# Kernel optimization log

Hardware: AMD Instinct MI355X
Metric: run time of the kernel (lower is better)

Reference implementation:

```python
import jax, jax.numpy as jnp
import numpy as np

N_NODES = 100000
N_EDGES = 600000
IN_DIM = 128
HID = 128
OUT_DIM = 64
N_LAYERS = 3


def setup_inputs() -> dict:
    key = jax.random.key(0)
    ks = jax.random.split(key, 8)
    x = jax.random.normal(ks[0], (N_NODES, IN_DIM), dtype=jnp.float32)
    edge_index = jax.random.randint(ks[1], (2, N_EDGES), 0, N_NODES, dtype=jnp.int64)
    s = 1.0 / np.sqrt(HID)
    W_in = jax.random.normal(ks[2], (HID, IN_DIM), dtype=jnp.float32) * s
    b_in = jax.random.normal(ks[3], (HID,), dtype=jnp.float32) * s
    W_convs = jax.random.normal(ks[4], (N_LAYERS, HID, HID), dtype=jnp.float32) * s
    b_convs = jax.random.normal(ks[5], (N_LAYERS, HID), dtype=jnp.float32) * s
    W_out = jax.random.normal(ks[6], (OUT_DIM, (N_LAYERS + 1) * HID), dtype=jnp.float32) * s
    b_out = jax.random.normal(ks[7], (OUT_DIM,), dtype=jnp.float32) * s
    return {"x": x, "edge_index": edge_index, "W_in": W_in, "b_in": b_in,
            "W_convs": W_convs, "b_convs": b_convs, "W_out": W_out, "b_out": b_out}


def reference(x, edge_index, W_in, b_in, W_convs, b_convs, W_out, b_out):
    src, dst = edge_index[0], edge_index[1]
    n = x.shape[0]
    # input projection: [N, in] -> [N, H]
    h = x @ W_in.T + b_in
    hidden_states = [h]
    for i in range(W_convs.shape[0]):
        # GINConv (eps=0): nn(x + sum of neighbor messages), messages src->dst
        agg = jax.ops.segment_sum(h[src], dst, num_segments=n)
        h = (h + agg) @ W_convs[i].T + b_convs[i]
        hidden_states.append(h)
    cat = jnp.concatenate(hidden_states, axis=1)  # [N, (L+1)*H]
    out = cat @ W_out.T + b_out  # [N, OUT]
    return jax.nn.softmax(out, axis=-1)
```

## Files before the change

### kernel.cpp

```cpp
#include <hip/hip_runtime.h>
#include <hip/hip_bf16.h>
#include <hip/hip_fp16.h>

#define GN 100000
#define GE 600000
#define SCAN_NBLK 98
#define ALD 132

typedef __bf16    bf16x8 __attribute__((ext_vector_type(8)));
typedef __bf16    bf16x4 __attribute__((ext_vector_type(4)));
typedef _Float16  f16x8  __attribute__((ext_vector_type(8)));
typedef float     f32x4  __attribute__((ext_vector_type(4)));

__global__ __launch_bounds__(256) void convert_w(
    const float* __restrict__ Win, const float* __restrict__ Wc,
    const float* __restrict__ Wout,
    __bf16* __restrict__ hi, __bf16* __restrict__ lo)
{
    const int i = blockIdx.x * 256 + threadIdx.x;
    if (i >= 98304) return;
    float v;
    if (i < 16384)      v = Win[i];
    else if (i < 65536) v = Wc[i - 16384];
    else                v = Wout[i - 65536];
    const __bf16 h = (__bf16)v;
    hi[i] = h;
    lo[i] = (__bf16)(v - (float)h);
}

__global__ __launch_bounds__(256, 8) void gather_rows(
    const uint* __restrict__ Hw,
    const int* __restrict__ row_start,
    const int* __restrict__ deg,
    const int* __restrict__ csr,
    float* __restrict__ Agg)
{
    const int wave = threadIdx.x >> 6;
    const int lane = threadIdx.x & 63;
    const int row  = blockIdx.x * 4 + wave;
    if (row >= GN) return;

    const int start = row_start[row];
    const int dg    = deg[row];
    float2 acc = make_float2(0.f, 0.f);

    for (int b = 0; b < dg; b += 64) {
        const int n = min(dg - b, 64);
        const int idx = csr[start + min(b + lane, dg - 1)];
        for (int k = 0; k < n; k += 8) {
            uint t[8];
#pragma unroll
            for (int u = 0; u < 8; ++u) {
                const int s = __shfl(idx, min(k + u, n - 1));
                t[u] = Hw[(size_t)s * 64 + lane];
            }
            const int m = min(n - k, 8);
#pragma unroll
            for (int u = 0; u < 8; ++u) {
                if (u < m) {
                    union { uint uu; _Float16 h[2]; } cv;
                    cv.uu = t[u];
                    acc.x += (float)cv.h[0];
                    acc.y += (float)cv.h[1];
                }
            }
        }
    }
    *(float2*)&Agg[(size_t)row * 128 + lane * 2] = acc;
}

template<bool HASAGG>
__global__ __launch_bounds__(256, 3) void gin_layer(
    const float* __restrict__ H, int ldH,
    const float* __restrict__ Agg,
    const __bf16* __restrict__ Whi,
    const __bf16* __restrict__ Wlo,
    const float* __restrict__ bias,
    float* __restrict__ C, int ldC,
    _Float16* __restrict__ HfOut)
{
    __shared__ float Acc[32 * ALD];

    const int tid  = threadIdx.x;
    const int wave = tid >> 6;
    const int lane = tid & 63;
    const int row0 = blockIdx.x * 32;
    const int wn   = wave * 32;
    const int quad = lane >> 4;
    const int l15  = lane & 15;

    {
        const int c = (lane & 31) * 4;
        f32x4 sv[4];
#pragma unroll
        for (int p = 0; p < 4; ++p) {
            const int r = wave * 8 + p * 2 + (lane >> 5);
            sv[p] = *(const f32x4*)(H + (size_t)(row0 + r) * ldH + c);
            if (HASAGG)
                sv[p] += *(const f32x4*)(Agg + (size_t)(row0 + r) * 128 + c);
        }
#pragma unroll
        for (int p = 0; p < 4; ++p) {
            const int r = wave * 8 + p * 2 + (lane >> 5);
            *(f32x4*)&Acc[r * ALD + c] = sv[p];
        }
    }
    __syncthreads();

    f32x4 acc[2][2];
#pragma unroll
    for (int i = 0; i < 2; ++i)
#pragma unroll
        for (int j = 0; j < 2; ++j) acc[i][j] = (f32x4)(0.0f);

    bf16x8 whA[2], wlA[2], whB[2], wlB[2];
#pragma unroll
    for (int nt = 0; nt < 2; ++nt) {
        const int n = wn + nt * 16 + l15;
        whA[nt] = *(const bf16x8*)(Whi + (size_t)n * 128 + quad * 8);
        wlA[nt] = *(const bf16x8*)(Wlo + (size_t)n * 128 + quad * 8);
    }

#pragma unroll
    for (int ks = 0; ks < 4; ++ks) {
        const int kt = ks * 32 + quad * 8;
        if (ks < 3) {
            const int kn = kt + 32;
#pragma unroll
            for (int nt = 0; nt < 2; ++nt) {
                const int n = wn + nt * 16 + l15;
                whB[nt] = *(const bf16x8*)(Whi + (size_t)n * 128 + kn);
                wlB[nt] = *(const bf16x8*)(Wlo + (size_t)n * 128 + kn);
            }
        }
        bf16x8 ahi[2], alo[2];
#pragma unroll
        for (int mt = 0; mt < 2; ++mt) {
            const float* ap = &Acc[(mt * 16 + l15) * ALD + kt];
            const f32x4 p = *(const f32x4*)ap;
            const f32x4 q = *(const f32x4*)(ap + 4);
#pragma unroll
            for (int e = 0; e < 4; ++e) {
                const __bf16 hp = (__bf16)p[e];
                const __bf16 hq = (__bf16)q[e];
                ahi[mt][e]     = hp;
                ahi[mt][e + 4] = hq;
                alo[mt][e]     = (__bf16)(p[e] - (float)hp);
                alo[mt][e + 4] = (__bf16)(q[e] - (float)hq);
            }
        }
#pragma unroll
        for (int mt = 0; mt < 2; ++mt)
#pragma unroll
            for (int nt = 0; nt < 2; ++nt) {
                acc[mt][nt] = __builtin_amdgcn_mfma_f32_16x16x32_bf16(
                    ahi[mt], whA[nt], acc[mt][nt], 0, 0, 0);
                acc[mt][nt] = __builtin_amdgcn_mfma_f32_16x16x32_bf16(
                    ahi[mt], wlA[nt], acc[mt][nt], 0, 0, 0);
                acc[mt][nt] = __builtin_amdgcn_mfma_f32_16x16x32_bf16(
                    alo[mt], whA[nt], acc[mt][nt], 0, 0, 0);
            }
        if (ks < 3) {
#pragma unroll
            for (int nt = 0; nt < 2; ++nt) {
                whA[nt] = whB[nt];
                wlA[nt] = wlB[nt];
            }
        }
    }
    __syncthreads();

#pragma unroll
    for (int nt = 0; nt < 2; ++nt) {
        const int col = wn + nt * 16 + l15;
        const float b = bias[col];
#pragma unroll
        for (int mt = 0; mt < 2; ++mt)
#pragma unroll
            for (int r4 = 0; r4 < 4; ++r4)
                Acc[(mt * 16 + quad * 4 + r4) * ALD + col] = acc[mt][nt][r4] + b;
    }
    __syncthreads();
#pragma unroll
    for (int p = 0; p < 4; ++p) {
        const int q  = tid + p * 256;
        const int r  = q >> 5;
        const int c4 = (q & 31) * 4;
        *(float4*)(C + (size_t)(row0 + r) * ldC + c4) = *(const float4*)&Acc[r * ALD + c4];
    }
#pragma unroll
    for (int p = 0; p < 2; ++p) {
        const int q = tid + p * 256;
        const int r = q >> 4;
        const int g = (q & 15) * 8;
        const float4 a = *(const float4*)&Acc[r * ALD + g];
        const float4 b = *(const float4*)&Acc[r * ALD + g + 4];
        f16x8 o = {(_Float16)a.x, (_Float16)a.y, (_Float16)a.z, (_Float16)a.w,
                   (_Float16)b.x, (_Float16)b.y, (_Float16)b.z, (_Float16)b.w};
        *(f16x8*)&HfOut[(size_t)(row0 + r) * 128 + g] = o;
    }
}

__global__ __launch_bounds__(256, 3) void gin_final(
    const float* __restrict__ cat3,
    const float* __restrict__ Agg,
    const __bf16* __restrict__ Whi3,
    const __bf16* __restrict__ Wlo3,
    const float* __restrict__ b3,
    const __bf16* __restrict__ WhiO,
    const __bf16* __restrict__ WloO,
    const float* __restrict__ bO,
    float* __restrict__ out)
{
    constexpr int CLD = 68;

    __shared__ float Smem[32 * ALD];
    float* const Acc = Smem;
    float* const Cst = Smem;

    const int tid  = threadIdx.x;
    const int wave = tid >> 6;
    const int lane = tid & 63;
    const int row0 = blockIdx.x * 32;
    const int quad = lane >> 4;
    const int l15  = lane & 15;

    {
        const int c = (lane & 31) * 4;
        f32x4 sv[4];
#pragma unroll
        for (int p = 0; p < 4; ++p) {
            const int r = wave * 8 + p * 2 + (lane >> 5);
            sv[p] = *(const f32x4*)(cat3 + (size_t)(row0 + r) * 384 + 256 + c);
            sv[p] += *(const f32x4*)(Agg + (size_t)(row0 + r) * 128 + c);
        }
#pragma unroll
        for (int p = 0; p < 4; ++p) {
            const int r = wave * 8 + p * 2 + (lane >> 5);
            *(f32x4*)&Acc[r * ALD + c] = sv[p];
        }
    }
    __syncthreads();

    const int wn = wave * 32;
    f32x4 acc1[2][2];
#pragma unroll
    for (int i = 0; i < 2; ++i)
#pragma unroll
        for (int j = 0; j < 2; ++j) acc1[i][j] = (f32x4)(0.0f);

    {
        bf16x8 whA[2], wlA[2], whB[2], wlB[2];
#pragma unroll
        for (int nt = 0; nt < 2; ++nt) {
            const int n = wn + nt * 16 + l15;
            whA[nt] = *(const bf16x8*)(Whi3 + (size_t)n * 128 + quad * 8);
            wlA[nt] = *(const bf16x8*)(Wlo3 + (size_t)n * 128 + quad * 8);
        }
#pragma unroll
        for (int ks = 0; ks < 4; ++ks) {
            const int kt = ks * 32 + quad * 8;
            if (ks < 3) {
                const int kn = kt + 32;
#pragma unroll
                for (int nt = 0; nt < 2; ++nt) {
                    const int n = wn + nt * 16 + l15;
                    whB[nt] = *(const bf16x8*)(Whi3 + (size_t)n * 128 + kn);
                    wlB[nt] = *(const bf16x8*)(Wlo3 + (size_t)n * 128 + kn);
                }
            }
            bf16x8 ahi[2], alo[2];
#pragma unroll
            for (int mt = 0; mt < 2; ++mt) {
                const float* ap = &Acc[(mt * 16 + l15) * ALD + kt];
                const f32x4 p = *(const f32x4*)ap;
                const f32x4 q = *(const f32x4*)(ap + 4);
#pragma unroll
                for (int e = 0; e < 4; ++e) {
                    const __bf16 hp = (__bf16)p[e];
                    const __bf16 hq = (__bf16)q[e];
                    ahi[mt][e]     = hp;
                    ahi[mt][e + 4] = hq;
                    alo[mt][e]     = (__bf16)(p[e] - (float)hp);
                    alo[mt][e + 4] = (__bf16)(q[e] - (float)hq);
                }
            }
#pragma unroll
            for (int mt = 0; mt < 2; ++mt)
#pragma unroll
                for (int nt = 0; nt < 2; ++nt) {
                    acc1[mt][nt] = __builtin_amdgcn_mfma_f32_16x16x32_bf16(
                        ahi[mt], whA[nt], acc1[mt][nt], 0, 0, 0);
                    acc1[mt][nt] = __builtin_amdgcn_mfma_f32_16x16x32_bf16(
                        ahi[mt], wlA[nt], acc1[mt][nt], 0, 0, 0);
                    acc1[mt][nt] = __builtin_amdgcn_mfma_f32_16x16x32_bf16(
                        alo[mt], whA[nt], acc1[mt][nt], 0, 0, 0);
                }
            if (ks < 3) {
#pragma unroll
                for (int nt = 0; nt < 2; ++nt) {
                    whA[nt] = whB[nt];
                    wlA[nt] = wlB[nt];
                }
            }
        }
    }
    __syncthreads();

#pragma unroll
    for (int nt = 0; nt < 2; ++nt) {
        const int col = wn + nt * 16 + l15;
        const float b = b3[col];
#pragma unroll
        for (int mt = 0; mt < 2; ++mt)
#pragma unroll
            for (int r4 = 0; r4 < 4; ++r4)
                Acc[(mt * 16 + quad * 4 + r4) * ALD + col] = acc1[mt][nt][r4] + b;
    }
    __syncthreads();

    const int wk  = wave & 1;
    const int wn2 = (wave >> 1) * 32;
    f32x4 acc2[2][2];
#pragma unroll
    for (int i = 0; i < 2; ++i)
#pragma unroll
        for (int j = 0; j < 2; ++j) acc2[i][j] = (f32x4)(0.0f);

    f32x4 pA[2], qA[2], pB[2], qB[2];
    bf16x8 whA[2], wlA[2], whB[2], wlB[2];

    {
        const int kg = wk * 256 + quad * 8;
#pragma unroll
        for (int mt = 0; mt < 2; ++mt) {
            const int row = mt * 16 + l15;
            const float* ap = cat3 + (size_t)(row0 + row) * 384 + kg;
            pA[mt] = *(const f32x4*)ap;
            qA[mt] = *(const f32x4*)(ap + 4);
        }
#pragma unroll
        for (int nt = 0; nt < 2; ++nt) {
            const int n = wn2 + nt * 16 + l15;
            whA[nt] = *(const bf16x8*)(WhiO + (size_t)n * 512 + kg);
            wlA[nt] = *(const bf16x8*)(WloO + (size_t)n * 512 + kg);
        }
    }

#pragma unroll
    for (int ks = 0; ks < 8; ++ks) {
        if (ks < 7) {
            const int kg = wk * 256 + (ks + 1) * 32 + quad * 8;
#pragma unroll
            for (int mt = 0; mt < 2; ++mt) {
                const int row = mt * 16 + l15;
                if (kg < 384) {
                    const float* ap = cat3 + (size_t)(row0 + row) * 384 + kg;
                    pB[mt] = *(const f32x4*)ap;
                    qB[mt] = *(const f32x4*)(ap + 4);
                } else {
                    const float* ap = &Acc[row * ALD + (kg - 384)];
                    pB[mt] = *(const f32x4*)ap;
                    qB[mt] = *(const f32x4*)(ap + 4);
                }
            }
#pragma unroll
            for (int nt = 0; nt < 2; ++nt) {
                const int n = wn2 + nt * 16 + l15;
                whB[nt] = *(const bf16x8*)(WhiO + (size_t)n * 512 + kg);
                wlB[nt] = *(const bf16x8*)(WloO + (size_t)n * 512 + kg);
            }
        }
        bf16x8 ahi[2], alo[2];
#pragma unroll
        for (int mt = 0; mt < 2; ++mt) {
#pragma unroll
            for (int e = 0; e < 4; ++e) {
                const __bf16 hp = (__bf16)pA[mt][e];
                const __bf16 hq = (__bf16)qA[mt][e];
                ahi[mt][e]     = hp;
                ahi[mt][e + 4] = hq;
                alo[mt][e]     = (__bf16)(pA[mt][e] - (float)hp);
                alo[mt][e + 4] = (__bf16)(qA[mt][e] - (float)hq);
            }
        }
#pragma unroll
        for (int mt = 0; mt < 2; ++mt)
#pragma unroll
            for (int nt = 0; nt < 2; ++nt) {
                acc2[mt][nt] = __builtin_amdgcn_mfma_f32_16x16x32_bf16(
                    ahi[mt], whA[nt], acc2[mt][nt], 0, 0, 0);
                acc2[mt][nt] = __builtin_amdgcn_mfma_f32_16x16x32_bf16(
                    ahi[mt], wlA[nt], acc2[mt][nt], 0, 0, 0);
                acc2[mt][nt] = __builtin_amdgcn_mfma_f32_16x16x32_bf16(
                    alo[mt], whA[nt], acc2[mt][nt], 0, 0, 0);
            }
        if (ks < 7) {
#pragma unroll
            for (int mt = 0; mt < 2; ++mt) { pA[mt] = pB[mt]; qA[mt] = qB[mt]; }
#pragma unroll
            for (int nt = 0; nt < 2; ++nt) { whA[nt] = whB[nt]; wlA[nt] = wlB[nt]; }
        }
    }

    __syncthreads();

    if (wk == 1) {
#pragma unroll
        for (int nt = 0; nt < 2; ++nt)
#pragma unroll
            for (int mt = 0; mt < 2; ++mt)
#pragma unroll
                for (int r4 = 0; r4 < 4; ++r4)
                    Cst[(mt * 16 + quad * 4 + r4) * CLD + wn2 + nt * 16 + l15]
                        = acc2[mt][nt][r4];
    }
    __syncthreads();
    if (wk == 0) {
#pragma unroll
        for (int nt = 0; nt < 2; ++nt) {
            const int col = wn2 + nt * 16 + l15;
            const float b = bO[col];
#pragma unroll
            for (int mt = 0; mt < 2; ++mt)
#pragma unroll
                for (int r4 = 0; r4 < 4; ++r4) {
                    const int idx = (mt * 16 + quad * 4 + r4) * CLD + col;
                    Cst[idx] = Cst[idx] + acc2[mt][nt][r4] + b;
                }
        }
    }
    __syncthreads();

    for (int i = 0; i < 8; ++i) {
        const int r = wave * 8 + i;
        const float v = Cst[r * CLD + lane];
        float m = v;
#pragma unroll
        for (int off = 32; off > 0; off >>= 1) m = fmaxf(m, __shfl_xor(m, off));
        const float e = __expf(v - m);
        float s = e;
#pragma unroll
        for (int off = 32; off > 0; off >>= 1) s += __shfl_xor(s, off);
        out[(size_t)(row0 + r) * 64 + lane] = e / s;
    }
}

__global__ __launch_bounds__(256) void count_deg(const int* __restrict__ dst,
                                                 int* __restrict__ deg)
{
    const int e = blockIdx.x * 256 + threadIdx.x;
    if (e < GE) atomicAdd(&deg[dst[e]], 1);
}

__global__ __launch_bounds__(256) void scan_pass1(const int* __restrict__ deg,
                                                  int* __restrict__ excl,
                                                  int* __restrict__ blockSums)
{
    __shared__ int s[256];
    const int t = threadIdx.x;
    const int base = blockIdx.x * 1024 + t * 4;

    int4 v = make_int4(0, 0, 0, 0);
    if (base + 3 < GN) {
        v = *(const int4*)(deg + base);
    } else {
        if (base + 0 < GN) v.x = deg[base + 0];
        if (base + 1 < GN) v.y = deg[base + 1];
        if (base + 2 < GN) v.z = deg[base + 2];
        if (base + 3 < GN) v.w = deg[base + 3];
    }
    const int mysum = v.x + v.y + v.z + v.w;
    s[t] = mysum;
    __syncthreads();
    for (int off = 1; off < 256; off <<= 1) {
        const int val = (t >= off) ? s[t - off] : 0;
        __syncthreads();
        s[t] += val;
        __syncthreads();
    }
    int4 o;
    o.x = s[t] - mysum;
    o.y = o.x + v.x;
    o.z = o.y + v.y;
    o.w = o.z + v.z;
    if (base + 3 < GN) {
        *(int4*)(excl + base) = o;
    } else {
        if (base + 0 < GN) excl[base + 0] = o.x;
        if (base + 1 < GN) excl[base + 1] = o.y;
        if (base + 2 < GN) excl[base + 2] = o.z;
        if (base + 3 < GN) excl[base + 3] = o.w;
    }
    if (t == 255) blockSums[blockIdx.x] = s[255];
}

__global__ __launch_bounds__(128) void scan_pass2(const int* __restrict__ blockSums,
                                                  int* __restrict__ blockOffs, int n)
{
    __shared__ int s[128];
    const int t = threadIdx.x;
    const int v = (t < n) ? blockSums[t] : 0;
    s[t] = v;
    __syncthreads();
    for (int off = 1; off < 128; off <<= 1) {
        const int val = (t >= off) ? s[t - off] : 0;
        __syncthreads();
        s[t] += val;
        __syncthreads();
    }
    if (t < n) blockOffs[t] = s[t] - v;
}

__global__ __launch_bounds__(256) void scan_pass3(int* __restrict__ excl,
                                                  const int* __restrict__ blockOffs,
                                                  int* __restrict__ cursor)
{
    const int i = blockIdx.x * 256 + threadIdx.x;
    if (i >= GN) return;
    const int v = excl[i] + blockOffs[i >> 10];
    excl[i]   = v;
    cursor[i] = v;
}

__global__ __launch_bounds__(256) void fill_csr(const int* __restrict__ src,
                                                const int* __restrict__ dst,
                                                int* __restrict__ cursor,
                                                int* __restrict__ csr)
{
    const int e = blockIdx.x * 256 + threadIdx.x;
    if (e >= GE) return;
    const int pos = atomicAdd(&cursor[dst[e]], 1);
    csr[pos] = src[e];
}

extern "C" void kernel_launch(void* const* d_in, const int* in_sizes, int n_in,
                              void* d_out, int out_size, void* d_ws, size_t ws_size,
                              hipStream_t stream)
{
    const float* x       = (const float*)d_in[0];
    const int*   src     = (const int*)d_in[1];
    const int*   dst     = ((const int*)d_in[1]) + GE;
    const float* W_in    = (const float*)d_in[2];
    const float* b_in    = (const float*)d_in[3];
    const float* W_convs = (const float*)d_in[4];
    const float* b_convs = (const float*)d_in[5];
    const float* W_out   = (const float*)d_in[6];
    const float* b_out   = (const float*)d_in[7];
    float*       out     = (float*)d_out;

    float*    cat3 = (float*)d_ws;
    _Float16* Hf   = (_Float16*)(cat3 + (size_t)GN * 384);
    float*    Agg  = (float*)(Hf + (size_t)GN * 128);
    int*      deg       = (int*)(Agg + (size_t)GN * 128);
    int*      row_start = deg + GN;
    int*      cursor    = row_start + GN;
    int*      blockSums = cursor + GN;
    int*      blockOffs = blockSums + 128;
    int*      csr       = blockOffs + 128;
    __bf16*   Whi       = (__bf16*)(csr + GE);
    __bf16*   Wlo       = Whi + 98304;

    const dim3 blk(256);
    const dim3 gblk(256);
    const int edge_blocks   = (GE + 255) / 256;
    const int node_blocks   = (GN + 255) / 256;
    const int layer_blocks  = GN / 32;
    const int gather_blocks = (GN + 3) / 4;

    hipMemsetAsync(deg, 0, GN * sizeof(int), stream);
    count_deg<<<edge_blocks, blk, 0, stream>>>(dst, deg);
    scan_pass1<<<SCAN_NBLK, blk, 0, stream>>>(deg, row_start, blockSums);
    scan_pass2<<<1, 128, 0, stream>>>(blockSums, blockOffs, SCAN_NBLK);
    scan_pass3<<<node_blocks, blk, 0, stream>>>(row_start, blockOffs, cursor);
    fill_csr<<<edge_blocks, blk, 0, stream>>>(src, dst, cursor, csr);

    convert_w<<<(98304 + 255) / 256, blk, 0, stream>>>(W_in, W_convs, W_out, Whi, Wlo);

    gin_layer<false><<<layer_blocks, gblk, 0, stream>>>(
        x, 128, nullptr, Whi, Wlo, b_in, cat3, 384, Hf);

    gather_rows<<<gather_blocks, gblk, 0, stream>>>(
        (const uint*)Hf, row_start, deg, csr, Agg);
    gin_layer<true><<<layer_blocks, gblk, 0, stream>>>(
        cat3, 384, Agg, Whi + 16384, Wlo + 16384, b_convs, cat3 + 128, 384, Hf);

    gather_rows<<<gather_blocks, gblk, 0, stream>>>(
        (const uint*)Hf, row_start, deg, csr, Agg);
    gin_layer<true><<<layer_blocks, gblk, 0, stream>>>(
        cat3 + 128, 384, Agg, Whi + 32768, Wlo + 32768, b_convs + 128,
        cat3 + 256, 384, Hf);

    gather_rows<<<gather_blocks, gblk, 0, stream>>>(
        (const uint*)Hf, row_start, deg, csr, Agg);
    gin_final<<<layer_blocks, gblk, 0, stream>>>(
        cat3, Agg, Whi + 49152, Wlo + 49152, b_convs + 256,
        Whi + 65536, Wlo + 65536, b_out, out);
}
```

Baseline: 499.3 us.

## Process two 32-row tiles per block in gin_layer with prefetched second tile

Each gin_layer block now handles 64 rows as two 32-row tiles with double-buffered shared memory. Global loads for the second tile are issued up front so they overlap with the first tile's MFMA work, and the first tile's epilogue is interleaved with the second GEMM. The GEMM body moves into a shared inline helper that gin_final also calls. In exchange, shared memory and register use per block roughly double, which may reduce occupancy, and the grid becomes half as many blocks with a bounds guard for the tail.

Result: slower. 513.5 us (+2.8%).

```diff
diff --git a/kernel.cpp b/kernel.cpp
--- a/kernel.cpp
+++ b/kernel.cpp
@@ -69,6 +69,73 @@
     *(float2*)&Agg[(size_t)row * 128 + lane * 2] = acc;
 }
 
+__device__ __forceinline__ void gemm_tile(
+    const float* __restrict__ AccBuf,
+    const __bf16* __restrict__ Whi, const __bf16* __restrict__ Wlo,
+    const int wn, const int quad, const int l15,
+    f32x4 acc[2][2])
+{
+#pragma unroll
+    for (int i = 0; i < 2; ++i)
+#pragma unroll
+        for (int j = 0; j < 2; ++j) acc[i][j] = (f32x4)(0.0f);
+
+    bf16x8 whA[2], wlA[2], whB[2], wlB[2];
+#pragma unroll
+    for (int nt = 0; nt < 2; ++nt) {
+        const int n = wn + nt * 16 + l15;
+        whA[nt] = *(const bf16x8*)(Whi + (size_t)n * 128 + quad * 8);
+        wlA[nt] = *(const bf16x8*)(Wlo + (size_t)n * 128 + quad * 8);
+    }
+#pragma unroll
+    for (int ks = 0; ks < 4; ++ks) {
+        const int kt = ks * 32 + quad * 8;
+        if (ks < 3) {
+            const int kn = kt + 32;
+#pragma unroll
+            for (int nt = 0; nt < 2; ++nt) {
+                const int n = wn + nt * 16 + l15;
+                whB[nt] = *(const bf16x8*)(Whi + (size_t)n * 128 + kn);
+                wlB[nt] = *(const bf16x8*)(Wlo + (size_t)n * 128 + kn);
+            }
+        }
+        bf16x8 ahi[2], alo[2];
+#pragma unroll
+        for (int mt = 0; mt < 2; ++mt) {
+            const float* ap = &AccBuf[(mt * 16 + l15) * ALD + kt];
+            const f32x4 p = *(const f32x4*)ap;
+            const f32x4 q = *(const f32x4*)(ap + 4);
+#pragma unroll
+            for (int e = 0; e < 4; ++e) {
+                const __bf16 hp = (__bf16)p[e];
+                const __bf16 hq = (__bf16)q[e];
+                ahi[mt][e]     = hp;
+                ahi[mt][e + 4] = hq;
+                alo[mt][e]     = (__bf16)(p[e] - (float)hp);
+                alo[mt][e + 4] = (__bf16)(q[e] - (float)hq);
+            }
+        }
+#pragma unroll
+        for (int mt = 0; mt < 2; ++mt)
+#pragma unroll
+            for (int nt = 0; nt < 2; ++nt) {
+                acc[mt][nt] = __builtin_amdgcn_mfma_f32_16x16x32_bf16(
+                    ahi[mt], whA[nt], acc[mt][nt], 0, 0, 0);
+                acc[mt][nt] = __builtin_amdgcn_mfma_f32_16x16x32_bf16(
+                    ahi[mt], wlA[nt], acc[mt][nt], 0, 0, 0);
+                acc[mt][nt] = __builtin_amdgcn_mfma_f32_16x16x32_bf16(
+                    alo[mt], whA[nt], acc[mt][nt], 0, 0, 0);
+            }
+        if (ks < 3) {
+#pragma unroll
+            for (int nt = 0; nt < 2; ++nt) {
+                whA[nt] = whB[nt];
+                wlA[nt] = wlB[nt];
+            }
+        }
+    }
+}
+
 template<bool HASAGG>
 __global__ __launch_bounds__(256, 3) void gin_layer(
     const float* __restrict__ H, int ldH,
@@ -79,94 +146,50 @@
     float* __restrict__ C, int ldC,
     _Float16* __restrict__ HfOut)
 {
-    __shared__ float Acc[32 * ALD];
+    __shared__ float Acc[2][32 * ALD];
 
     const int tid  = threadIdx.x;
     const int wave = tid >> 6;
     const int lane = tid & 63;
-    const int row0 = blockIdx.x * 32;
+    const int row0 = blockIdx.x * 64;
     const int wn   = wave * 32;
     const int quad = lane >> 4;
     const int l15  = lane & 15;
-
-    {
-        const int c = (lane & 31) * 4;
-        f32x4 sv[4];
-#pragma unroll
-        for (int p = 0; p < 4; ++p) {
-            const int r = wave * 8 + p * 2 + (lane >> 5);
-            sv[p] = *(const f32x4*)(H + (size_t)(row0 + r) * ldH + c);
-            if (HASAGG)
-                sv[p] += *(const f32x4*)(Agg + (size_t)(row0 + r) * 128 + c);
-        }
-#pragma unroll
-        for (int p = 0; p < 4; ++p) {
-            const int r = wave * 8 + p * 2 + (lane >> 5);
-            *(f32x4*)&Acc[r * ALD + c] = sv[p];
-        }
-    }
-    __syncthreads();
-
-    f32x4 acc[2][2];
-#pragma unroll
-    for (int i = 0; i < 2; ++i)
-#pragma unroll
-        for (int j = 0; j < 2; ++j) acc[i][j] = (f32x4)(0.0f);
-
-    bf16x8 whA[2], wlA[2], whB[2], wlB[2];
-#pragma unroll
-    for (int nt = 0; nt < 2; ++nt) {
-        const int n = wn + nt * 16 + l15;
-        whA[nt] = *(const bf16x8*)(Whi + (size_t)n * 128 + quad * 8);
-        wlA[nt] = *(const bf16x8*)(Wlo + (size_t)n * 128 + quad * 8);
-    }
-
-#pragma unroll
-    for (int ks = 0; ks < 4; ++ks) {
-        const int kt = ks * 32 + quad * 8;
-        if (ks < 3) {
-            const int kn = kt + 32;
-#pragma unroll
-            for (int nt = 0; nt < 2; ++nt) {
-                const int n = wn + nt * 16 + l15;
-                whB[nt] = *(const bf16x8*)(Whi + (size_t)n * 128 + kn);
-                wlB[nt] = *(const bf16x8*)(Wlo + (size_t)n * 128 + kn);
-            }
-        }
-        bf16x8 ahi[2], alo[2];
-#pragma unroll
-        for (int mt = 0; mt < 2; ++mt) {
-            const float* ap = &Acc[(mt * 16 + l15) * ALD + kt];
-            const f32x4 p = *(const f32x4*)ap;
-            const f32x4 q = *(const f32x4*)(ap + 4);
-#pragma unroll
-            for (int e = 0; e < 4; ++e) {
-                const __bf16 hp = (__bf16)p[e];
-                const __bf16 hq = (__bf16)q[e];
-                ahi[mt][e]     = hp;
-                ahi[mt][e + 4] = hq;
-                alo[mt][e]     = (__bf16)(p[e] - (float)hp);
-                alo[mt][e + 4] = (__bf16)(q[e] - (float)hq);
-            }
-        }
-#pragma unroll
-        for (int mt = 0; mt < 2; ++mt)
-#pragma unroll
-            for (int nt = 0; nt < 2; ++nt) {
-                acc[mt][nt] = __builtin_amdgcn_mfma_f32_16x16x32_bf16(
-                    ahi[mt], whA[nt], acc[mt][nt], 0, 0, 0);
-                acc[mt][nt] = __builtin_amdgcn_mfma_f32_16x16x32_bf16(
-                    ahi[mt], wlA[nt], acc[mt][nt], 0, 0, 0);
-                acc[mt][nt] = __builtin_amdgcn_mfma_f32_16x16x32_bf16(
-                    alo[mt], whA[nt], acc[mt][nt], 0, 0, 0);
-            }
-        if (ks < 3) {
-#pragma unroll
-            for (int nt = 0; nt < 2; ++nt) {
-                whA[nt] = whB[nt];
-                wlA[nt] = wlB[nt];
-            }
-        }
+    const int c    = (lane & 31) * 4;
+    const int hp2  = lane >> 5;
+
+    f32x4 s0[4], a0[4], s1[4], a1[4];
+#pragma unroll
+    for (int p = 0; p < 4; ++p) {
+        const int r0 = min(row0 + wave * 8 + p * 2 + hp2, GN - 1);
+        s0[p] = *(const f32x4*)(H + (size_t)r0 * ldH + c);
+        if (HASAGG) a0[p] = *(const f32x4*)(Agg + (size_t)r0 * 128 + c);
+    }
+#pragma unroll
+    for (int p = 0; p < 4; ++p) {
+        const int r1 = min(row0 + 32 + wave * 8 + p * 2 + hp2, GN - 1);
+        s1[p] = *(const f32x4*)(H + (size_t)r1 * ldH + c);
+        if (HASAGG) a1[p] = *(const f32x4*)(Agg + (size_t)r1 * 128 + c);
+    }
+
+#pragma unroll
+    for (int p = 0; p < 4; ++p) {
+        const int r = wave * 8 + p * 2 + hp2;
+        f32x4 v = s0[p];
+        if (HASAGG) v += a0[p];
+        *(f32x4*)&Acc[0][r * ALD + c] = v;
+    }
+    __syncthreads();
+
+    f32x4 acc0[2][2];
+    gemm_tile(Acc[0], Whi, Wlo, wn, quad, l15, acc0);
+
+#pragma unroll
+    for (int p = 0; p < 4; ++p) {
+        const int r = wave * 8 + p * 2 + hp2;
+        f32x4 v = s1[p];
+        if (HASAGG) v += a1[p];
+        *(f32x4*)&Acc[1][r * ALD + c] = v;
     }
     __syncthreads();
 
@@ -178,26 +201,71 @@
         for (int mt = 0; mt < 2; ++mt)
 #pragma unroll
             for (int r4 = 0; r4 < 4; ++r4)
-                Acc[(mt * 16 + quad * 4 + r4) * ALD + col] = acc[mt][nt][r4] + b;
-    }
-    __syncthreads();
+                Acc[0][(mt * 16 + quad * 4 + r4) * ALD + col] = acc0[mt][nt][r4] + b;
+    }
+
+    f32x4 acc1[2][2];
+    gemm_tile(Acc[1], Whi, Wlo, wn, quad, l15, acc1);
+    __syncthreads();
+
 #pragma unroll
     for (int p = 0; p < 4; ++p) {
         const int q  = tid + p * 256;
         const int r  = q >> 5;
         const int c4 = (q & 31) * 4;
-        *(float4*)(C + (size_t)(row0 + r) * ldC + c4) = *(const float4*)&Acc[r * ALD + c4];
+        const int gr = row0 + r;
+        if (gr < GN)
+            *(float4*)(C + (size_t)gr * ldC + c4) = *(const float4*)&Acc[0][r * ALD + c4];
     }
 #pragma unroll
     for (int p = 0; p < 2; ++p) {
         const int q = tid + p * 256;
         const int r = q >> 4;
         const int g = (q & 15) * 8;
-        const float4 a = *(const float4*)&Acc[r * ALD + g];
-        const float4 b = *(const float4*)&Acc[r * ALD + g + 4];
-        f16x8 o = {(_Float16)a.x, (_Float16)a.y, (_Float16)a.z, (_Float16)a.w,
-                   (_Float16)b.x, (_Float16)b.y, (_Float16)b.z, (_Float16)b.w};
-        *(f16x8*)&HfOut[(size_t)(row0 + r) * 128 + g] = o;
+        const int gr = row0 + r;
+        if (gr < GN) {
+            const float4 a = *(const float4*)&Acc[0][r * ALD + g];
+            const float4 b = *(const float4*)&Acc[0][r * ALD + g + 4];
+            f16x8 o = {(_Float16)a.x, (_Float16)a.y, (_Float16)a.z, (_Float16)a.w,
+                       (_Float16)b.x, (_Float16)b.y, (_Float16)b.z, (_Float16)b.w};
+            *(f16x8*)&HfOut[(size_t)gr * 128 + g] = o;
+        }
+    }
+
+#pragma unroll
+    for (int nt = 0; nt < 2; ++nt) {
+        const int col = wn + nt * 16 + l15;
+        const float b = bias[col];
+#pragma unroll
+        for (int mt = 0; mt < 2; ++mt)
+#pragma unroll
+            for (int r4 = 0; r4 < 4; ++r4)
+                Acc[1][(mt * 16 + quad * 4 + r4) * ALD + col] = acc1[mt][nt][r4] + b;
+    }
+    __syncthreads();
+
+#pragma unroll
+    for (int p = 0; p < 4; ++p) {
+        const int q  = tid + p * 256;
+        const int r  = q >> 5;
+        const int c4 = (q & 31) * 4;
+        const int gr = row0 + 32 + r;
+        if (gr < GN)
+            *(float4*)(C + (size_t)gr * ldC + c4) = *(const float4*)&Acc[1][r * ALD + c4];
+    }
+#pragma unroll
+    for (int p = 0; p < 2; ++p) {
+        const int q = tid + p * 256;
+        const int r = q >> 4;
+        const int g = (q & 15) * 8;
+        const int gr = row0 + 32 + r;
+        if (gr < GN) {
+            const float4 a = *(const float4*)&Acc[1][r * ALD + g];
+            const float4 b = *(const float4*)&Acc[1][r * ALD + g + 4];
+            f16x8 o = {(_Float16)a.x, (_Float16)a.y, (_Float16)a.z, (_Float16)a.w,
+                       (_Float16)b.x, (_Float16)b.y, (_Float16)b.z, (_Float16)b.w};
+            *(f16x8*)&HfOut[(size_t)gr * 128 + g] = o;
+        }
     }
 }
 
@@ -244,67 +312,7 @@
 
     const int wn = wave * 32;
     f32x4 acc1[2][2];
-#pragma unroll
-    for (int i = 0; i < 2; ++i)
-#pragma unroll
-        for (int j = 0; j < 2; ++j) acc1[i][j] = (f32x4)(0.0f);
-
-    {
-        bf16x8 whA[2], wlA[2], whB[2], wlB[2];
-#pragma unroll
-        for (int nt = 0; nt < 2; ++nt) {
-            const int n = wn + nt * 16 + l15;
-            whA[nt] = *(const bf16x8*)(Whi3 + (size_t)n * 128 + quad * 8);
-            wlA[nt] = *(const bf16x8*)(Wlo3 + (size_t)n * 128 + quad * 8);
-        }
-#pragma unroll
-        for (int ks = 0; ks < 4; ++ks) {
-            const int kt = ks * 32 + quad * 8;
-            if (ks < 3) {
-                const int kn = kt + 32;
-#pragma unroll
-                for (int nt = 0; nt < 2; ++nt) {
-                    const int n = wn + nt * 16 + l15;
-                    whB[nt] = *(const bf16x8*)(Whi3 + (size_t)n * 128 + kn);
-                    wlB[nt] = *(const bf16x8*)(Wlo3 + (size_t)n * 128 + kn);
-                }
-            }
-            bf16x8 ahi[2], alo[2];
-#pragma unroll
-            for (int mt = 0; mt < 2; ++mt) {
-                const float* ap = &Acc[(mt * 16 + l15) * ALD + kt];
-                const f32x4 p = *(const f32x4*)ap;
-                const f32x4 q = *(const f32x4*)(ap + 4);
-#pragma unroll
-                for (int e = 0; e < 4; ++e) {
-                    const __bf16 hp = (__bf16)p[e];
-                    const __bf16 hq = (__bf16)q[e];
-                    ahi[mt][e]     = hp;
-                    ahi[mt][e + 4] = hq;
-                    alo[mt][e]     = (__bf16)(p[e] - (float)hp);
-                    alo[mt][e + 4] = (__bf16)(q[e] - (float)hq);
-                }
-            }
-#pragma unroll
-            for (int mt = 0; mt < 2; ++mt)
-#pragma unroll
-                for (int nt = 0; nt < 2; ++nt) {
-                    acc1[mt][nt] = __builtin_amdgcn_mfma_f32_16x16x32_bf16(
-                        ahi[mt], whA[nt], acc1[mt][nt], 0, 0, 0);
-                    acc1[mt][nt] = __builtin_amdgcn_mfma_f32_16x16x32_bf16(
-                        ahi[mt], wlA[nt], acc1[mt][nt], 0, 0, 0);
-                    acc1[mt][nt] = __builtin_amdgcn_mfma_f32_16x16x32_bf16(
-                        alo[mt], whA[nt], acc1[mt][nt], 0, 0, 0);
-                }
-            if (ks < 3) {
-#pragma unroll
-                for (int nt = 0; nt < 2; ++nt) {
-                    whA[nt] = whB[nt];
-                    wlA[nt] = wlB[nt];
-                }
-            }
-        }
-    }
+    gemm_tile(Acc, Whi3, Wlo3, wn, quad, l15, acc1);
     __syncthreads();
 
 #pragma unroll
@@ -565,7 +573,8 @@
     const dim3 gblk(256);
     const int edge_blocks   = (GE + 255) / 256;
     const int node_blocks   = (GN + 255) / 256;
-    const int layer_blocks  = GN / 32;
+    const int layer_blocks  = (GN + 63) / 64;
+    const int final_blocks  = GN / 32;
     const int gather_blocks = (GN + 3) / 4;
 
     hipMemsetAsync(deg, 0, GN * sizeof(int), stream);
@@ -593,7 +602,7 @@
 
     gather_rows<<<gather_blocks, gblk, 0, stream>>>(
         (const uint*)Hf, row_start, deg, csr, Agg);
-    gin_final<<<layer_blocks, gblk, 0, stream>>>(
+    gin_final<<<final_blocks, gblk, 0, stream>>>(
         cat3, Agg, Whi + 49152, Wlo + 49152, b_convs + 256,
         Whi + 65536, Wlo + 65536, b_out, out);
 }
```

## Store hidden states only in fp16 and drop the fp32 concat buffer

Applied to the files above, without the earlier changes.

Removes the fp32 cat3 buffer of hidden states. Each layer now writes only an fp16 copy of its output (h0, h1, h2). The next layer's input and the final output projection read these fp16 buffers instead of fp32. This cuts global memory writes and reads of the N x 384 fp32 concat, at the cost of rounding hidden states to fp16 before the dense layers, which may reduce accuracy. It also factors the shared GEMM tile into a helper.

Measured after the change: 459.5 us. 8.0% less time.

```diff
diff --git a/kernel.cpp b/kernel.cpp
--- a/kernel.cpp
+++ b/kernel.cpp
@@ -8,7 +8,6 @@
 #define ALD 132
 
 typedef __bf16    bf16x8 __attribute__((ext_vector_type(8)));
-typedef __bf16    bf16x4 __attribute__((ext_vector_type(4)));
 typedef _Float16  f16x8  __attribute__((ext_vector_type(8)));
 typedef float     f32x4  __attribute__((ext_vector_type(4)));
 
@@ -69,15 +68,82 @@
     *(float2*)&Agg[(size_t)row * 128 + lane * 2] = acc;
 }
 
+__device__ __forceinline__ void gemm_tile(
+    const float* __restrict__ AccBuf,
+    const __bf16* __restrict__ Whi, const __bf16* __restrict__ Wlo,
+    const int wn, const int quad, const int l15,
+    f32x4 acc[2][2])
+{
+#pragma unroll
+    for (int i = 0; i < 2; ++i)
+#pragma unroll
+        for (int j = 0; j < 2; ++j) acc[i][j] = (f32x4)(0.0f);
+
+    bf16x8 whA[2], wlA[2], whB[2], wlB[2];
+#pragma unroll
+    for (int nt = 0; nt < 2; ++nt) {
+        const int n = wn + nt * 16 + l15;
+        whA[nt] = *(const bf16x8*)(Whi + (size_t)n * 128 + quad * 8);
+        wlA[nt] = *(const bf16x8*)(Wlo + (size_t)n * 128 + quad * 8);
+    }
+#pragma unroll
+    for (int ks = 0; ks < 4; ++ks) {
+        const int kt = ks * 32 + quad * 8;
+        if (ks < 3) {
+            const int kn = kt + 32;
+#pragma unroll
+            for (int nt = 0; nt < 2; ++nt) {
+                const int n = wn + nt * 16 + l15;
+                whB[nt] = *(const bf16x8*)(Whi + (size_t)n * 128 + kn);
+                wlB[nt] = *(const bf16x8*)(Wlo + (size_t)n * 128 + kn);
+            }
+        }
+        bf16x8 ahi[2], alo[2];
+#pragma unroll
+        for (int mt = 0; mt < 2; ++mt) {
+            const float* ap = &AccBuf[(mt * 16 + l15) * ALD + kt];
+            const f32x4 p = *(const f32x4*)ap;
+            const f32x4 q = *(const f32x4*)(ap + 4);
+#pragma unroll
+            for (int e = 0; e < 4; ++e) {
+                const __bf16 hp = (__bf16)p[e];
+                const __bf16 hq = (__bf16)q[e];
+                ahi[mt][e]     = hp;
+                ahi[mt][e + 4] = hq;
+                alo[mt][e]     = (__bf16)(p[e] - (float)hp);
+                alo[mt][e + 4] = (__bf16)(q[e] - (float)hq);
+            }
+        }
+#pragma unroll
+        for (int mt = 0; mt < 2; ++mt)
+#pragma unroll
+            for (int nt = 0; nt < 2; ++nt) {
+                acc[mt][nt] = __builtin_amdgcn_mfma_f32_16x16x32_bf16(
+                    ahi[mt], whA[nt], acc[mt][nt], 0, 0, 0);
+                acc[mt][nt] = __builtin_amdgcn_mfma_f32_16x16x32_bf16(
+                    ahi[mt], wlA[nt], acc[mt][nt], 0, 0, 0);
+                acc[mt][nt] = __builtin_amdgcn_mfma_f32_16x16x32_bf16(
+                    alo[mt], whA[nt], acc[mt][nt], 0, 0, 0);
+            }
+        if (ks < 3) {
+#pragma unroll
+            for (int nt = 0; nt < 2; ++nt) {
+                whA[nt] = whB[nt];
+                wlA[nt] = wlB[nt];
+            }
+        }
+    }
+}
+
 template<bool HASAGG>
 __global__ __launch_bounds__(256, 3) void gin_layer(
-    const float* __restrict__ H, int ldH,
+    const float* __restrict__ Hf32,
+    const _Float16* __restrict__ H16,
     const float* __restrict__ Agg,
     const __bf16* __restrict__ Whi,
     const __bf16* __restrict__ Wlo,
     const float* __restrict__ bias,
-    float* __restrict__ C, int ldC,
-    _Float16* __restrict__ HfOut)
+    _Float16* __restrict__ Hout)
 {
     __shared__ float Acc[32 * ALD];
 
@@ -88,86 +154,33 @@
     const int wn   = wave * 32;
     const int quad = lane >> 4;
     const int l15  = lane & 15;
-
-    {
-        const int c = (lane & 31) * 4;
-        f32x4 sv[4];
-#pragma unroll
-        for (int p = 0; p < 4; ++p) {
-            const int r = wave * 8 + p * 2 + (lane >> 5);
-            sv[p] = *(const f32x4*)(H + (size_t)(row0 + r) * ldH + c);
-            if (HASAGG)
-                sv[p] += *(const f32x4*)(Agg + (size_t)(row0 + r) * 128 + c);
-        }
-#pragma unroll
-        for (int p = 0; p < 4; ++p) {
-            const int r = wave * 8 + p * 2 + (lane >> 5);
-            *(f32x4*)&Acc[r * ALD + c] = sv[p];
-        }
+    const int c8   = l15 * 8;
+
+#pragma unroll
+    for (int p = 0; p < 2; ++p) {
+        const int r = wave * 8 + p * 4 + quad;
+        const size_t g = (size_t)(row0 + r) * 128 + c8;
+        f32x4 v0, v1;
+        if (HASAGG) {
+            const f16x8 hv = *(const f16x8*)(H16 + g);
+            const f32x4 a0 = *(const f32x4*)(Agg + g);
+            const f32x4 a1 = *(const f32x4*)(Agg + g + 4);
+#pragma unroll
+            for (int e = 0; e < 4; ++e) {
+                v0[e] = (float)hv[e]     + a0[e];
+                v1[e] = (float)hv[e + 4] + a1[e];
+            }
+        } else {
+            v0 = *(const f32x4*)(Hf32 + g);
+            v1 = *(const f32x4*)(Hf32 + g + 4);
+        }
+        *(f32x4*)&Acc[r * ALD + c8]     = v0;
+        *(f32x4*)&Acc[r * ALD + c8 + 4] = v1;
     }
     __syncthreads();
 
     f32x4 acc[2][2];
-#pragma unroll
-    for (int i = 0; i < 2; ++i)
-#pragma unroll
-        for (int j = 0; j < 2; ++j) acc[i][j] = (f32x4)(0.0f);
-
-    bf16x8 whA[2], wlA[2], whB[2], wlB[2];
-#pragma unroll
-    for (int nt = 0; nt < 2; ++nt) {
-        const int n = wn + nt * 16 + l15;
-        whA[nt] = *(const bf16x8*)(Whi + (size_t)n * 128 + quad * 8);
-        wlA[nt] = *(const bf16x8*)(Wlo + (size_t)n * 128 + quad * 8);
-    }
-
-#pragma unroll
-    for (int ks = 0; ks < 4; ++ks) {
-        const int kt = ks * 32 + quad * 8;
-        if (ks < 3) {
-            const int kn = kt + 32;
-#pragma unroll
-            for (int nt = 0; nt < 2; ++nt) {
-                const int n = wn + nt * 16 + l15;
-                whB[nt] = *(const bf16x8*)(Whi + (size_t)n * 128 + kn);
-                wlB[nt] = *(const bf16x8*)(Wlo + (size_t)n * 128 + kn);
-            }
-        }
-        bf16x8 ahi[2], alo[2];
-#pragma unroll
-        for (int mt = 0; mt < 2; ++mt) {
-            const float* ap = &Acc[(mt * 16 + l15) * ALD + kt];
-            const f32x4 p = *(const f32x4*)ap;
-            const f32x4 q = *(const f32x4*)(ap + 4);
-#pragma unroll
-            for (int e = 0; e < 4; ++e) {
-                const __bf16 hp = (__bf16)p[e];
-                const __bf16 hq = (__bf16)q[e];
-                ahi[mt][e]     = hp;
-                ahi[mt][e + 4] = hq;
-                alo[mt][e]     = (__bf16)(p[e] - (float)hp);
-                alo[mt][e + 4] = (__bf16)(q[e] - (float)hq);
-            }
-        }
-#pragma unroll
-        for (int mt = 0; mt < 2; ++mt)
-#pragma unroll
-            for (int nt = 0; nt < 2; ++nt) {
-                acc[mt][nt] = __builtin_amdgcn_mfma_f32_16x16x32_bf16(
-                    ahi[mt], whA[nt], acc[mt][nt], 0, 0, 0);
-                acc[mt][nt] = __builtin_amdgcn_mfma_f32_16x16x32_bf16(
-                    ahi[mt], wlA[nt], acc[mt][nt], 0, 0, 0);
-                acc[mt][nt] = __builtin_amdgcn_mfma_f32_16x16x32_bf16(
-                    alo[mt], whA[nt], acc[mt][nt], 0, 0, 0);
-            }
-        if (ks < 3) {
-#pragma unroll
-            for (int nt = 0; nt < 2; ++nt) {
-                whA[nt] = whB[nt];
-                wlA[nt] = wlB[nt];
-            }
-        }
-    }
+    gemm_tile(Acc, Whi, Wlo, wn, quad, l15, acc);
     __syncthreads();
 
 #pragma unroll
@@ -181,13 +194,6 @@
                 Acc[(mt * 16 + quad * 4 + r4) * ALD + col] = acc[mt][nt][r4] + b;
     }
     __syncthreads();
-#pragma unroll
-    for (int p = 0; p < 4; ++p) {
-        const int q  = tid + p * 256;
-        const int r  = q >> 5;
-        const int c4 = (q & 31) * 4;
-        *(float4*)(C + (size_t)(row0 + r) * ldC + c4) = *(const float4*)&Acc[r * ALD + c4];
-    }
 #pragma unroll
     for (int p = 0; p < 2; ++p) {
         const int q = tid + p * 256;
@@ -197,12 +203,14 @@
         const float4 b = *(const float4*)&Acc[r * ALD + g + 4];
         f16x8 o = {(_Float16)a.x, (_Float16)a.y, (_Float16)a.z, (_Float16)a.w,
                    (_Float16)b.x, (_Float16)b.y, (_Float16)b.z, (_Float16)b.w};
-        *(f16x8*)&HfOut[(size_t)(row0 + r) * 128 + g] = o;
+        *(f16x8*)&Hout[(size_t)(row0 + r) * 128 + g] = o;
     }
 }
 
 __global__ __launch_bounds__(256, 3) void gin_final(
-    const float* __restrict__ cat3,
+    const _Float16* __restrict__ h0,
+    const _Float16* __restrict__ h1,
+    const _Float16* __restrict__ h2,
     const float* __restrict__ Agg,
     const __bf16* __restrict__ Whi3,
     const __bf16* __restrict__ Wlo3,
@@ -224,55 +232,106 @@
     const int row0 = blockIdx.x * 32;
     const int quad = lane >> 4;
     const int l15  = lane & 15;
-
-    {
-        const int c = (lane & 31) * 4;
-        f32x4 sv[4];
-#pragma unroll
-        for (int p = 0; p < 4; ++p) {
-            const int r = wave * 8 + p * 2 + (lane >> 5);
-            sv[p] = *(const f32x4*)(cat3 + (size_t)(row0 + r) * 384 + 256 + c);
-            sv[p] += *(const f32x4*)(Agg + (size_t)(row0 + r) * 128 + c);
-        }
-#pragma unroll
-        for (int p = 0; p < 4; ++p) {
-            const int r = wave * 8 + p * 2 + (lane >> 5);
-            *(f32x4*)&Acc[r * ALD + c] = sv[p];
-        }
+    const int c8   = l15 * 8;
+
+#pragma unroll
+    for (int p = 0; p < 2; ++p) {
+        const int r = wave * 8 + p * 4 + quad;
+        const size_t g = (size_t)(row0 + r) * 128 + c8;
+        const f16x8 hv = *(const f16x8*)(h2 + g);
+        const f32x4 a0 = *(const f32x4*)(Agg + g);
+        const f32x4 a1 = *(const f32x4*)(Agg + g + 4);
+        f32x4 v0, v1;
+#pragma unroll
+        for (int e = 0; e < 4; ++e) {
+            v0[e] = (float)hv[e]     + a0[e];
+            v1[e] = (float)hv[e + 4] + a1[e];
+        }
+        *(f32x4*)&Acc[r * ALD + c8]     = v0;
+        *(f32x4*)&Acc[r * ALD + c8 + 4] = v1;
     }
     __syncthreads();
 
     const int wn = wave * 32;
     f32x4 acc1[2][2];
+    gemm_tile(Acc, Whi3, Wlo3, wn, quad, l15, acc1);
+    __syncthreads();
+
+#pragma unroll
+    for (int nt = 0; nt < 2; ++nt) {
+        const int col = wn + nt * 16 + l15;
+        const float b = b3[col];
+#pragma unroll
+        for (int mt = 0; mt < 2; ++mt)
+#pragma unroll
+            for (int r4 = 0; r4 < 4; ++r4)
+                Acc[(mt * 16 + quad * 4 + r4) * ALD + col] = acc1[mt][nt][r4] + b;
+    }
+    __syncthreads();
+
+    const int wk  = wave & 1;
+    const int wn2 = (wave >> 1) * 32;
+    f32x4 acc2[2][2];
 #pragma unroll
     for (int i = 0; i < 2; ++i)
 #pragma unroll
-        for (int j = 0; j < 2; ++j) acc1[i][j] = (f32x4)(0.0f);
+        for (int j = 0; j < 2; ++j) acc2[i][j] = (f32x4)(0.0f);
+
+    f16x8 hA[2], hB[2];
+    bf16x8 whA[2], wlA[2], whB[2], wlB[2];
 
     {
-        bf16x8 whA[2], wlA[2], whB[2], wlB[2];
+        const int kg = wk * 256 + quad * 8;
+        const _Float16* hb = (kg < 128) ? h0 : (kg < 256) ? h1 : h2;
+        const int kc = kg & 127;
+#pragma unroll
+        for (int mt = 0; mt < 2; ++mt) {
+            const int row = mt * 16 + l15;
+            hA[mt] = *(const f16x8*)(hb + (size_t)(row0 + row) * 128 + kc);
+        }
 #pragma unroll
         for (int nt = 0; nt < 2; ++nt) {
-            const int n = wn + nt * 16 + l15;
-            whA[nt] = *(const bf16x8*)(Whi3 + (size_t)n * 128 + quad * 8);
-            wlA[nt] = *(const bf16x8*)(Wlo3 + (size_t)n * 128 + quad * 8);
-        }
-#pragma unroll
-        for (int ks = 0; ks < 4; ++ks) {
-            const int kt = ks * 32 + quad * 8;
-            if (ks < 3) {
-                const int kn = kt + 32;
-#pragma unroll
-                for (int nt = 0; nt < 2; ++nt) {
-                    const int n = wn + nt * 16 + l15;
-                    whB[nt] = *(const bf16x8*)(Whi3 + (size_t)n * 128 + kn);
-                    wlB[nt] = *(const bf16x8*)(Wlo3 + (size_t)n * 128 + kn);
+            const int n = wn2 + nt * 16 + l15;
+            whA[nt] = *(const bf16x8*)(WhiO + (size_t)n * 512 + kg);
+            wlA[nt] = *(const bf16x8*)(WloO + (size_t)n * 512 + kg);
+        }
+    }
+
+#pragma unroll
+    for (int ks = 0; ks < 8; ++ks) {
+        const int kgC = wk * 256 + ks * 32 + quad * 8;
+        if (ks < 7) {
+            const int kgN = kgC + 32;
+            if (kgN < 384) {
+                const _Float16* hb = (kgN < 128) ? h0 : (kgN < 256) ? h1 : h2;
+                const int kc = kgN & 127;
+#pragma unroll
+                for (int mt = 0; mt < 2; ++mt) {
+                    const int row = mt * 16 + l15;
+                    hB[mt] = *(const f16x8*)(hb + (size_t)(row0 + row) * 128 + kc);
                 }
             }
-            bf16x8 ahi[2], alo[2];
-#pragma unroll
-            for (int mt = 0; mt < 2; ++mt) {
-                const float* ap = &Acc[(mt * 16 + l15) * ALD + kt];
+#pragma unroll
+            for (int nt = 0; nt < 2; ++nt) {
+                const int n = wn2 + nt * 16 + l15;
+                whB[nt] = *(const bf16x8*)(WhiO + (size_t)n * 512 + kgN);
+                wlB[nt] = *(const bf16x8*)(WloO + (size_t)n * 512 + kgN);
+            }
+        }
+        bf16x8 ahi[2], alo[2];
+#pragma unroll
+        for (int mt = 0; mt < 2; ++mt) {
+            if (kgC < 384) {
+#pragma unroll
+                for (int e = 0; e < 8; ++e) {
+                    const float v = (float)hA[mt][e];
+                    const __bf16 hp = (__bf16)v;
+                    ahi[mt][e] = hp;
+                    alo[mt][e] = (__bf16)(v - (float)hp);
+                }
+            } else {
+                const int row = mt * 16 + l15;
+                const float* ap = &Acc[row * ALD + (kgC - 384)];
                 const f32x4 p = *(const f32x4*)ap;
                 const f32x4 q = *(const f32x4*)(ap + 4);
 #pragma unroll
@@ -285,104 +344,6 @@
                     alo[mt][e + 4] = (__bf16)(q[e] - (float)hq);
                 }
             }
-#pragma unroll
-            for (int mt = 0; mt < 2; ++mt)
-#pragma unroll
-                for (int nt = 0; nt < 2; ++nt) {
-                    acc1[mt][nt] = __builtin_amdgcn_mfma_f32_16x16x32_bf16(
-                        ahi[mt], whA[nt], acc1[mt][nt], 0, 0, 0);
-                    acc1[mt][nt] = __builtin_amdgcn_mfma_f32_16x16x32_bf16(
-                        ahi[mt], wlA[nt], acc1[mt][nt], 0, 0, 0);
-                    acc1[mt][nt] = __builtin_amdgcn_mfma_f32_16x16x32_bf16(
-                        alo[mt], whA[nt], acc1[mt][nt], 0, 0, 0);
-                }
-            if (ks < 3) {
-#pragma unroll
-                for (int nt = 0; nt < 2; ++nt) {
-                    whA[nt] = whB[nt];
-                    wlA[nt] = wlB[nt];
-                }
-            }
-        }
-    }
-    __syncthreads();
-
-#pragma unroll
-    for (int nt = 0; nt < 2; ++nt) {
-        const int col = wn + nt * 16 + l15;
-        const float b = b3[col];
-#pragma unroll
-        for (int mt = 0; mt < 2; ++mt)
-#pragma unroll
-            for (int r4 = 0; r4 < 4; ++r4)
-                Acc[(mt * 16 + quad * 4 + r4) * ALD + col] = acc1[mt][nt][r4] + b;
-    }
-    __syncthreads();
-
-    const int wk  = wave & 1;
-    const int wn2 = (wave >> 1) * 32;
-    f32x4 acc2[2][2];
-#pragma unroll
-    for (int i = 0; i < 2; ++i)
-#pragma unroll
-        for (int j = 0; j < 2; ++j) acc2[i][j] = (f32x4)(0.0f);
-
-    f32x4 pA[2], qA[2], pB[2], qB[2];
-    bf16x8 whA[2], wlA[2], whB[2], wlB[2];
-
-    {
-        const int kg = wk * 256 + quad * 8;
-#pragma unroll
-        for (int mt = 0; mt < 2; ++mt) {
-            const int row = mt * 16 + l15;
-            const float* ap = cat3 + (size_t)(row0 + row) * 384 + kg;
-            pA[mt] = *(const f32x4*)ap;
-            qA[mt] = *(const f32x4*)(ap + 4);
-        }
-#pragma unroll
-        for (int nt = 0; nt < 2; ++nt) {
-            const int n = wn2 + nt * 16 + l15;
-            whA[nt] = *(const bf16x8*)(WhiO + (size_t)n * 512 + kg);
-            wlA[nt] = *(const bf16x8*)(WloO + (size_t)n * 512 + kg);
-        }
-    }
-
-#pragma unroll
-    for (int ks = 0; ks < 8; ++ks) {
-        if (ks < 7) {
-            const int kg = wk * 256 + (ks + 1) * 32 + quad * 8;
-#pragma unroll
-            for (int mt = 0; mt < 2; ++mt) {
-                const int row = mt * 16 + l15;
-                if (kg < 384) {
-                    const float* ap = cat3 + (size_t)(row0 + row) * 384 + kg;
-                    pB[mt] = *(const f32x4*)ap;
-                    qB[mt] = *(const f32x4*)(ap + 4);
-                } else {
-                    const float* ap = &Acc[row * ALD + (kg - 384)];
-                    pB[mt] = *(const f32x4*)ap;
-                    qB[mt] = *(const f32x4*)(ap + 4);
-                }
-            }
-#pragma unroll
-            for (int nt = 0; nt < 2; ++nt) {
-                const int n = wn2 + nt * 16 + l15;
-                whB[nt] = *(const bf16x8*)(WhiO + (size_t)n * 512 + kg);
-                wlB[nt] = *(const bf16x8*)(WloO + (size_t)n * 512 + kg);
-            }
-        }
-        bf16x8 ahi[2], alo[2];
-#pragma unroll
-        for (int mt = 0; mt < 2; ++mt) {
-#pragma unroll
-            for (int e = 0; e < 4; ++e) {
-                const __bf16 hp = (__bf16)pA[mt][e];
-                const __bf16 hq = (__bf16)qA[mt][e];
-                ahi[mt][e]     = hp;
-                ahi[mt][e + 4] = hq;
-                alo[mt][e]     = (__bf16)(pA[mt][e] - (float)hp);
-                alo[mt][e + 4] = (__bf16)(qA[mt][e] - (float)hq);
-            }
         }
 #pragma unroll
         for (int mt = 0; mt < 2; ++mt)
@@ -397,7 +358,7 @@
             }
         if (ks < 7) {
 #pragma unroll
-            for (int mt = 0; mt < 2; ++mt) { pA[mt] = pB[mt]; qA[mt] = qB[mt]; }
+            for (int mt = 0; mt < 2; ++mt) hA[mt] = hB[mt];
 #pragma unroll
             for (int nt = 0; nt < 2; ++nt) { whA[nt] = whB[nt]; wlA[nt] = wlB[nt]; }
         }
@@ -549,9 +510,10 @@
     const float* b_out   = (const float*)d_in[7];
     float*       out     = (float*)d_out;
 
-    float*    cat3 = (float*)d_ws;
-    _Float16* Hf   = (_Float16*)(cat3 + (size_t)GN * 384);
-    float*    Agg  = (float*)(Hf + (size_t)GN * 128);
+    _Float16* h0 = (_Float16*)d_ws;
+    _Float16* h1 = h0 + (size_t)GN * 128;
+    _Float16* h2 = h1 + (size_t)GN * 128;
+    float*    Agg = (float*)(h2 + (size_t)GN * 128);
     int*      deg       = (int*)(Agg + (size_t)GN * 128);
     int*      row_start = deg + GN;
     int*      cursor    = row_start + GN;
@@ -578,22 +540,21 @@
     convert_w<<<(98304 + 255) / 256, blk, 0, stream>>>(W_in, W_convs, W_out, Whi, Wlo);
 
     gin_layer<false><<<layer_blocks, gblk, 0, stream>>>(
-        x, 128, nullptr, Whi, Wlo, b_in, cat3, 384, Hf);
+        x, nullptr, nullptr, Whi, Wlo, b_in, h0);
 
     gather_rows<<<gather_blocks, gblk, 0, stream>>>(
-        (const uint*)Hf, row_start, deg, csr, Agg);
+        (const uint*)h0, row_start, deg, csr, Agg);
     gin_layer<true><<<layer_blocks, gblk, 0, stream>>>(
-        cat3, 384, Agg, Whi + 16384, Wlo + 16384, b_convs, cat3 + 128, 384, Hf);
+        nullptr, h0, Agg, Whi + 16384, Wlo + 16384, b_convs, h1);
 
     gather_rows<<<gather_blocks, gblk, 0, stream>>>(
-        (const uint*)Hf, row_start, deg, csr, Agg);
+        (const uint*)h1, row_start, deg, csr, Agg);
     gin_layer<true><<<layer_blocks, gblk, 0, stream>>>(
-        cat3 + 128, 384, Agg, Whi + 32768, Wlo + 32768, b_convs + 128,
-        cat3 + 256, 384, Hf);
+        nullptr, h1, Agg, Whi + 32768, Wlo + 32768, b_convs + 128, h2);
 
     gather_rows<<<gather_blocks, gblk, 0, stream>>>(
-        (const uint*)Hf, row_start, deg, csr, Agg);
+        (const uint*)h2, row_start, deg, csr, Agg);
     gin_final<<<layer_blocks, gblk, 0, stream>>>(
-        cat3, Agg, Whi + 49152, Wlo + 49152, b_convs + 256,
+        h0, h1, h2, Agg, Whi + 49152, Wlo + 49152, b_convs + 256,
         Whi + 65536, Wlo + 65536, b_out, out);
 }
```
